# Optimization experiments

Measured on AMD Instinct MI355X. Metric: run time of the kernel, lower is better.

Reference implementation:

```python
import jax, jax.numpy as jnp
import numpy as np

N = 100000   # nodes
E = 1600000  # edges (avg degree 16)
F_IN, F_HID, F_OUT = 64, 64, 16


def setup_inputs() -> dict:
    key = jax.random.key(0)
    ks = jax.random.split(key, 10)
    features = jax.random.normal(ks[0], (N, F_IN), dtype=jnp.float32)
    src = jax.random.randint(ks[1], (E,), 0, N, dtype=jnp.int32)
    dst = jax.random.randint(ks[2], (E,), 0, N, dtype=jnp.int32)
    # Xavier-uniform weights, zero bias (matches nn.init in the module)
    def xavier(k, fan_in, fan_out):
        lim = np.sqrt(6.0 / (fan_in + fan_out))
        return jax.random.uniform(k, (fan_in, fan_out), jnp.float32, -lim, lim)
    return {
        "features": features,
        "W1": xavier(ks[3], F_IN, F_HID), "b1": jnp.zeros((F_HID,), jnp.float32),
        "W2": xavier(ks[4], F_HID, F_HID), "b2": jnp.zeros((F_HID,), jnp.float32),
        "W3": xavier(ks[5], F_HID, F_OUT), "b3": jnp.zeros((F_OUT,), jnp.float32),
        "src": src, "dst": dst,
    }


def pairnorm_scs(x):
    # PairNorm 'PN-SCS', scale=1
    col_mean = x.mean(axis=0)                                    # [F]
    rownorm = jnp.sqrt(1e-6 + jnp.sum(x * x, axis=1, keepdims=True))  # [N,1]
    return x / rownorm - col_mean


def graph_conv(h, src, dst, W, b):
    # copy_u('h','m') + sum reduce over edges, plus self-loop
    agg = jax.ops.segment_sum(h[src], dst, num_segments=N) + h   # [N,F]
    return agg @ W + b


def reference(features, W1, b1, W2, b2, W3, b3, src, dst):
    h = features
    for W, b in ((W1, b1), (W2, b2)):
        h = pairnorm_scs(h)
        h = jax.nn.relu(graph_conv(h, src, dst, W, b))
        # dropout p=0.0 -> identity
    return graph_conv(h, src, dst, W3, b3)
```

## Files before the change

kernel.cpp:

```cpp
#include <hip/hip_runtime.h>


#define NHB 64

__device__ __forceinline__ unsigned short f2bf(float f) {
  unsigned u = __builtin_bit_cast(unsigned, f);
  u += 0x7FFFu + ((u >> 16) & 1u);
  return (unsigned short)(u >> 16);
}
__device__ __forceinline__ float bf2f(unsigned short h) {
  return __builtin_bit_cast(float, ((unsigned)h) << 16);
}

__global__ __launch_bounds__(256) void prelude_kernel(
    const int* __restrict__ dst, int* __restrict__ cntA, int E,
    const float* __restrict__ x, float* __restrict__ cs, int n4) {
  __shared__ int lc[NHB];
  __shared__ float lds[16][64];
  const int t = threadIdx.x;
  if (t < NHB) lc[t] = 0;
  __syncthreads();
  const int stride = gridDim.x * blockDim.x;
  for (int e = blockIdx.x * blockDim.x + t; e < E; e += stride)
    atomicAdd(&lc[__builtin_nontemporal_load(&dst[e]) >> 11], 1);

  float s0 = 0.f, s1 = 0.f, s2 = 0.f, s3 = 0.f;
  for (int i = blockIdx.x * blockDim.x + t; i < n4; i += stride) {
    float4 v = ((const float4*)x)[i];
    s0 += v.x; s1 += v.y; s2 += v.z; s3 += v.w;
  }
  const int r = t >> 4;
  const int cq = (t & 15) * 4;
  lds[r][cq + 0] = s0; lds[r][cq + 1] = s1; lds[r][cq + 2] = s2; lds[r][cq + 3] = s3;
  __syncthreads();
  if (t < NHB && lc[t]) atomicAdd(&cntA[t], lc[t]);
  if (t < 64) {
    float tot = 0.f;
    #pragma unroll
    for (int rr = 0; rr < 16; ++rr) tot += lds[rr][t];
    unsafeAtomicAdd(&cs[t], tot);
  }
}

__global__ void colsum_kernel(const float* __restrict__ x, float* __restrict__ cs,
                              int n4) {
  __shared__ float lds[16][64];
  float s0 = 0.f, s1 = 0.f, s2 = 0.f, s3 = 0.f;
  const int t = threadIdx.x;
  const int stride = gridDim.x * blockDim.x;
  for (int i = blockIdx.x * blockDim.x + t; i < n4; i += stride) {
    float4 v = ((const float4*)x)[i];
    s0 += v.x; s1 += v.y; s2 += v.z; s3 += v.w;
  }
  const int r = t >> 4;
  const int cq = (t & 15) * 4;
  lds[r][cq + 0] = s0; lds[r][cq + 1] = s1; lds[r][cq + 2] = s2; lds[r][cq + 3] = s3;
  __syncthreads();
  if (t < 64) {
    float tot = 0.f;
    #pragma unroll
    for (int rr = 0; rr < 16; ++rr) tot += lds[rr][t];
    unsafeAtomicAdd(&cs[t], tot);
  }
}

__global__ __launch_bounds__(256) void matnorm_kernel(
    const float* x, const float* __restrict__ W,
    const float* __restrict__ cs, unsigned short* __restrict__ z,
    int N, float invN) {
  const int lane = threadIdx.x & 63;
  const int wid  = blockIdx.x * (blockDim.x >> 6) + (threadIdx.x >> 6);
  const int nw   = gridDim.x * (blockDim.x >> 6);

  float w[64];
  float cm = 0.f;
  #pragma unroll
  for (int k = 0; k < 64; ++k) {
    w[k] = W[k * 64 + lane];
    cm = fmaf(cs[k], w[k], cm);
  }
  cm *= invN;

  for (int row = wid; row < N; row += nw) {
    const float xv = x[(size_t)row * 64 + lane];
    float ss = xv * xv;
    #pragma unroll
    for (int m = 1; m < 64; m <<= 1) ss += __shfl_xor(ss, m, 64);
    const float rinv = 1.0f / sqrtf(1e-6f + ss);
    float acc = 0.f;
    #pragma unroll
    for (int k = 0; k < 64; ++k) {
      const float xk = __builtin_bit_cast(
          float, __builtin_amdgcn_readlane(__builtin_bit_cast(int, xv), k));
      acc = fmaf(xk, w[k], acc);
    }
    z[(size_t)row * 64 + lane] = f2bf(acc * rinv - cm);
  }
}

__global__ __launch_bounds__(256) void mat16_kernel(
    const float* __restrict__ x, const float* __restrict__ W3,
    unsigned short* __restrict__ z3, int N) {
  const int lane = threadIdx.x & 63;
  const int j = lane & 15;
  const int wid = blockIdx.x * (blockDim.x >> 6) + (threadIdx.x >> 6);
  const int nw  = gridDim.x * (blockDim.x >> 6);

  float w[64];
  #pragma unroll
  for (int k = 0; k < 64; ++k) w[k] = W3[k * 16 + j];
  for (int row = wid; row < N; row += nw) {
    const float xv = x[(size_t)row * 64 + lane];
    float acc = 0.f;
    #pragma unroll
    for (int k = 0; k < 64; ++k) {
      const float xk = __builtin_bit_cast(
          float, __builtin_amdgcn_readlane(__builtin_bit_cast(int, xv), k));
      acc = fmaf(xk, w[k], acc);
    }
    if (lane < 16) z3[(size_t)row * 16 + lane] = f2bf(acc);
  }
}


__global__ void scanA_kernel(const int* __restrict__ cntA,
                             int* __restrict__ baseA, int* __restrict__ curA,
                             int NHI) {
  if (threadIdx.x == 0) {
    int acc = 0;
    for (int p = 0; p < NHI; ++p) { baseA[p] = acc; curA[p] = acc; acc += cntA[p]; }
    baseA[NHI] = acc;
  }
}

#define TILE 2048
#define CAPA 96
__global__ __launch_bounds__(256) void scatterA_kernel(
    const int* __restrict__ src, const int* __restrict__ dst,
    int* __restrict__ curA, int* __restrict__ psrc, int* __restrict__ pdst,
    int E) {
  __shared__ int lss[NHB][CAPA], ldd[NHB][CAPA];
  __shared__ int lcnt[NHB], lbase[NHB];
  const int t = threadIdx.x;
  if (t < NHB) lcnt[t] = 0;
  __syncthreads();
  const int ntiles = (E + TILE - 1) / TILE;
  for (int tile = blockIdx.x; tile < ntiles; tile += gridDim.x) {
    const int base = tile * TILE;
    #pragma unroll
    for (int j = 0; j < TILE / 256; ++j) {
      const int e = base + j * 256 + t;
      if (e < E) {
        const int d = __builtin_nontemporal_load(&dst[e]);
        const int s = __builtin_nontemporal_load(&src[e]);
        const int p = d >> 11;
        const int slot = atomicAdd(&lcnt[p], 1);
        if (slot < CAPA) { lss[p][slot] = s; ldd[p][slot] = d; }
        else {
          const int pos = atomicAdd(&curA[p], 1);
          psrc[pos] = s; pdst[pos] = d;
        }
      }
    }
    __syncthreads();
    if (t < NHB) {
      int c = lcnt[t]; if (c > CAPA) c = CAPA;
      lbase[t] = c ? atomicAdd(&curA[t], c) : 0;
      lcnt[t] = c;
    }
    __syncthreads();
    for (int p = 0; p < NHB; ++p) {
      const int c = lcnt[p];
      if (t < c) {
        psrc[lbase[p] + t] = lss[p][t];
        pdst[lbase[p] + t] = ldd[p][t];
      }
    }
    __syncthreads();
    if (t < NHB) lcnt[t] = 0;
    __syncthreads();
  }
}

__global__ __launch_bounds__(1024) void fillsort_kernel(
    const int* __restrict__ psrc, const int* __restrict__ pdst,
    const int* __restrict__ baseA, int* __restrict__ rowstart,
    int* __restrict__ csr, int N, int E) {
  __shared__ int hist[2048];
  __shared__ int bs[1024];
  const int t = threadIdx.x;
  const int h = blockIdx.x;
  const int nlo = h << 11;
  const int elo = baseA[h], ehi = baseA[h + 1];

  for (int i = t; i < 2048; i += 1024) hist[i] = 0;
  __syncthreads();

  int e = elo + t;
  for (; e + 3 * 1024 < ehi; e += 4 * 1024) {
    const int d0 = pdst[e], d1 = pdst[e + 1024],
              d2 = pdst[e + 2048], d3 = pdst[e + 3072];
    atomicAdd(&hist[d0 - nlo], 1); atomicAdd(&hist[d1 - nlo], 1);
    atomicAdd(&hist[d2 - nlo], 1); atomicAdd(&hist[d3 - nlo], 1);
  }
  for (; e < ehi; e += 1024) atomicAdd(&hist[pdst[e] - nlo], 1);
  __syncthreads();

  const int c0 = hist[2 * t], c1 = hist[2 * t + 1];
  const int s = c0 + c1;
  bs[t] = s;
  __syncthreads();
  for (int off = 1; off < 1024; off <<= 1) {
    const int v = (t >= off) ? bs[t - off] : 0;
    __syncthreads();
    bs[t] += v;
    __syncthreads();
  }
  const int excl = bs[t] - s;

  const int n0 = nlo + 2 * t;
  hist[2 * t] = excl;
  hist[2 * t + 1] = excl + c0;
  if (n0 < N)     rowstart[n0]     = elo + excl;
  if (n0 + 1 < N) rowstart[n0 + 1] = elo + excl + c0;
  if (h == 0 && t == 0) rowstart[N] = E;
  __syncthreads();

  e = elo + t;
  for (; e + 3 * 1024 < ehi; e += 4 * 1024) {
    const int d0 = pdst[e],        s0 = psrc[e];
    const int d1 = pdst[e + 1024], s1 = psrc[e + 1024];
    const int d2 = pdst[e + 2048], s2 = psrc[e + 2048];
    const int d3 = pdst[e + 3072], s3 = psrc[e + 3072];
    csr[elo + atomicAdd(&hist[d0 - nlo], 1)] = s0;
    csr[elo + atomicAdd(&hist[d1 - nlo], 1)] = s1;
    csr[elo + atomicAdd(&hist[d2 - nlo], 1)] = s2;
    csr[elo + atomicAdd(&hist[d3 - nlo], 1)] = s3;
  }
  for (; e < ehi; e += 1024) {
    const int d = pdst[e], sv = psrc[e];
    csr[elo + atomicAdd(&hist[d - nlo], 1)] = sv;
  }
}

__global__ __launch_bounds__(256) void gather64_kernel(
    const unsigned short* __restrict__ z, const float* __restrict__ b,
    const int* __restrict__ rowstart, const int* __restrict__ csr,
    float* __restrict__ agg, int N) {
  const int lane = threadIdx.x & 63;
  int node = blockIdx.x * (blockDim.x >> 6) + (threadIdx.x >> 6);
  if (node >= N) return;
  node = __builtin_amdgcn_readfirstlane(node);
  const int start = rowstart[node];
  const int end   = rowstart[node + 1];
  const unsigned short hs = z[(size_t)node * 64 + lane];
  float a0 = 0.f, a1 = 0.f, a2 = 0.f, a3 = 0.f;
  int e = start;
  for (; e + 16 <= end; e += 16) {
    unsigned short h[16];
    #pragma unroll
    for (int j = 0; j < 16; ++j) h[j] = z[(size_t)csr[e + j] * 64 + lane];
    #pragma unroll
    for (int j = 0; j < 16; j += 4) {
      a0 += bf2f(h[j + 0]); a1 += bf2f(h[j + 1]);
      a2 += bf2f(h[j + 2]); a3 += bf2f(h[j + 3]);
    }
  }
  for (; e + 4 <= end; e += 4) {
    unsigned short h[4];
    #pragma unroll
    for (int j = 0; j < 4; ++j) h[j] = z[(size_t)csr[e + j] * 64 + lane];
    a0 += bf2f(h[0]); a1 += bf2f(h[1]); a2 += bf2f(h[2]); a3 += bf2f(h[3]);
  }
  for (; e < end; ++e) a0 += bf2f(z[(size_t)csr[e] * 64 + lane]);
  const float sum = (a0 + a1) + (a2 + a3);
  agg[(size_t)node * 64 + lane] = fmaxf(bf2f(hs) + b[lane] + sum, 0.f);
}

__global__ __launch_bounds__(256) void gather16_kernel(
    const unsigned short* __restrict__ z3, const float* __restrict__ b3,
    const int* __restrict__ rowstart, const int* __restrict__ csr,
    float* __restrict__ out, int N) {
  const int lane = threadIdx.x & 63;
  const int f = lane & 15;
  const int g = lane >> 4;
  int node = blockIdx.x * (blockDim.x >> 6) + (threadIdx.x >> 6);
  if (node >= N) return;
  node = __builtin_amdgcn_readfirstlane(node);
  const int start = rowstart[node];
  const int end   = rowstart[node + 1];
  float acc0 = 0.f, acc1 = 0.f;
  int e = start + g;
  for (; e + 4 < end; e += 8) {
    acc0 += bf2f(z3[(size_t)csr[e] * 16 + f]);
    acc1 += bf2f(z3[(size_t)csr[e + 4] * 16 + f]);
  }
  if (e < end) acc0 += bf2f(z3[(size_t)csr[e] * 16 + f]);
  float acc = acc0 + acc1;
  acc += __shfl_xor(acc, 16, 64);
  acc += __shfl_xor(acc, 32, 64);
  if (lane < 16)
    out[(size_t)node * 16 + f] = bf2f(z3[(size_t)node * 16 + f]) + b3[f] + acc;
}

extern "C" void kernel_launch(void* const* d_in, const int* in_sizes, int n_in,
                              void* d_out, int out_size, void* d_ws, size_t ws_size,
                              hipStream_t stream) {
  const float* feat = (const float*)d_in[0];
  const float* W1 = (const float*)d_in[1];
  const float* b1 = (const float*)d_in[2];
  const float* W2 = (const float*)d_in[3];
  const float* b2 = (const float*)d_in[4];
  const float* W3 = (const float*)d_in[5];
  const float* b3 = (const float*)d_in[6];
  const int* src = (const int*)d_in[7];
  const int* dst = (const int*)d_in[8];
  const int N = in_sizes[0] / 64;
  const int E = in_sizes[7];
  float* out = (float*)d_out;

  float* B            = (float*)d_ws;
  unsigned short* zb  = (unsigned short*)(B + (size_t)N * 64);
  unsigned short* z3b = zb + (size_t)N * 64;
  int* cntA  = (int*)(z3b + (size_t)N * 16);
  float* cs1 = (float*)(cntA + NHB);
  float* cs2 = cs1 + 64;
  int* baseA    = (int*)(cs2 + 64);
  int* curA     = baseA + NHB + 1;
  int* rowstart = curA + NHB;
  int* csr      = rowstart + N + 1;
  int* psrc = (int*)zb;
  int* pdst = psrc + E;

  const int NHI = (N + 2047) >> 11;
  const int node_blocks = (N + 3) / 4;
  const float invN = 1.0f / (float)N;

  hipMemsetAsync(cntA, 0, (NHB + 128) * sizeof(int), stream);
  prelude_kernel<<<512, 256, 0, stream>>>(dst, cntA, E, feat, cs1, N * 16);
  scanA_kernel<<<1, 64, 0, stream>>>(cntA, baseA, curA, NHI);
  scatterA_kernel<<<512, 256, 0, stream>>>(src, dst, curA, psrc, pdst, E);
  fillsort_kernel<<<NHI, 1024, 0, stream>>>(psrc, pdst, baseA, rowstart, csr, N, E);

  matnorm_kernel<<<1024, 256, 0, stream>>>(feat, W1, cs1, zb, N, invN);
  gather64_kernel<<<node_blocks, 256, 0, stream>>>(zb, b1, rowstart, csr, B, N);

  colsum_kernel<<<512, 256, 0, stream>>>(B, cs2, N * 16);
  matnorm_kernel<<<1024, 256, 0, stream>>>(B, W2, cs2, zb, N, invN);
  gather64_kernel<<<node_blocks, 256, 0, stream>>>(zb, b2, rowstart, csr, B, N);

  mat16_kernel<<<1024, 256, 0, stream>>>(B, W3, z3b, N);
  gather16_kernel<<<node_blocks, 256, 0, stream>>>(z3b, b3, rowstart, csr, out, N);
}
```

Before: 426.0 us.

## Fuse layer-1 aggregation with layer-2 normalize/matmul and pack edge keys

The column-mean correction is moved out of the pre-aggregation term and applied after aggregation as degree+1 times (mean·W), which lets each layer's gather kernel also do the next layer's row normalization and matmul. The separate colsum, matnorm and mat16 passes disappear, and so do the fp32 intermediate writes and reads. The edge partition also packs src and the low dst bits into one 32-bit word, halving scatter traffic. In exchange the fused kernels reload W from global per node, and the packing assumes src fits in 21 bits.

Measured after the change: 524.1 us. 1.23x slower.

```diff
diff --git a/kernel.cpp b/kernel.cpp
--- a/kernel.cpp
+++ b/kernel.cpp
@@ -42,44 +42,33 @@
   }
 }
 
-__global__ void colsum_kernel(const float* __restrict__ x, float* __restrict__ cs,
-                              int n4) {
-  __shared__ float lds[16][64];
-  float s0 = 0.f, s1 = 0.f, s2 = 0.f, s3 = 0.f;
+__global__ void scanA_kernel(const int* __restrict__ cntA,
+                             int* __restrict__ baseA, int* __restrict__ curA,
+                             const float* __restrict__ cs1,
+                             const float* __restrict__ W1,
+                             float* __restrict__ cmW1, int NHI, float invN) {
   const int t = threadIdx.x;
-  const int stride = gridDim.x * blockDim.x;
-  for (int i = blockIdx.x * blockDim.x + t; i < n4; i += stride) {
-    float4 v = ((const float4*)x)[i];
-    s0 += v.x; s1 += v.y; s2 += v.z; s3 += v.w;
-  }
-  const int r = t >> 4;
-  const int cq = (t & 15) * 4;
-  lds[r][cq + 0] = s0; lds[r][cq + 1] = s1; lds[r][cq + 2] = s2; lds[r][cq + 3] = s3;
-  __syncthreads();
-  if (t < 64) {
-    float tot = 0.f;
-    #pragma unroll
-    for (int rr = 0; rr < 16; ++rr) tot += lds[rr][t];
-    unsafeAtomicAdd(&cs[t], tot);
-  }
+  if (t == 0) {
+    int acc = 0;
+    for (int p = 0; p < NHI; ++p) { baseA[p] = acc; curA[p] = acc; acc += cntA[p]; }
+    baseA[NHI] = acc;
+  }
+  float cm = 0.f;
+  #pragma unroll
+  for (int k = 0; k < 64; ++k) cm = fmaf(cs1[k], W1[k * 64 + t], cm);
+  cmW1[t] = cm * invN;
 }
 
 __global__ __launch_bounds__(256) void matnorm_kernel(
-    const float* x, const float* __restrict__ W,
-    const float* __restrict__ cs, unsigned short* __restrict__ z,
-    int N, float invN) {
+    const float* __restrict__ x, const float* __restrict__ W,
+    unsigned short* __restrict__ z, int N) {
   const int lane = threadIdx.x & 63;
   const int wid  = blockIdx.x * (blockDim.x >> 6) + (threadIdx.x >> 6);
   const int nw   = gridDim.x * (blockDim.x >> 6);
 
   float w[64];
-  float cm = 0.f;
   #pragma unroll
-  for (int k = 0; k < 64; ++k) {
-    w[k] = W[k * 64 + lane];
-    cm = fmaf(cs[k], w[k], cm);
-  }
-  cm *= invN;
+  for (int k = 0; k < 64; ++k) w[k] = W[k * 64 + lane];
 
   for (int row = wid; row < N; row += nw) {
     const float xv = x[(size_t)row * 64 + lane];
@@ -94,52 +83,17 @@
           float, __builtin_amdgcn_readlane(__builtin_bit_cast(int, xv), k));
       acc = fmaf(xk, w[k], acc);
     }
-    z[(size_t)row * 64 + lane] = f2bf(acc * rinv - cm);
-  }
-}
-
-__global__ __launch_bounds__(256) void mat16_kernel(
-    const float* __restrict__ x, const float* __restrict__ W3,
-    unsigned short* __restrict__ z3, int N) {
-  const int lane = threadIdx.x & 63;
-  const int j = lane & 15;
-  const int wid = blockIdx.x * (blockDim.x >> 6) + (threadIdx.x >> 6);
-  const int nw  = gridDim.x * (blockDim.x >> 6);
-
-  float w[64];
-  #pragma unroll
-  for (int k = 0; k < 64; ++k) w[k] = W3[k * 16 + j];
-  for (int row = wid; row < N; row += nw) {
-    const float xv = x[(size_t)row * 64 + lane];
-    float acc = 0.f;
-    #pragma unroll
-    for (int k = 0; k < 64; ++k) {
-      const float xk = __builtin_bit_cast(
-          float, __builtin_amdgcn_readlane(__builtin_bit_cast(int, xv), k));
-      acc = fmaf(xk, w[k], acc);
-    }
-    if (lane < 16) z3[(size_t)row * 16 + lane] = f2bf(acc);
-  }
-}
-
-
-__global__ void scanA_kernel(const int* __restrict__ cntA,
-                             int* __restrict__ baseA, int* __restrict__ curA,
-                             int NHI) {
-  if (threadIdx.x == 0) {
-    int acc = 0;
-    for (int p = 0; p < NHI; ++p) { baseA[p] = acc; curA[p] = acc; acc += cntA[p]; }
-    baseA[NHI] = acc;
-  }
-}
+    z[(size_t)row * 64 + lane] = f2bf(acc * rinv);
+  }
+}
+
 
 #define TILE 2048
 #define CAPA 96
 __global__ __launch_bounds__(256) void scatterA_kernel(
     const int* __restrict__ src, const int* __restrict__ dst,
-    int* __restrict__ curA, int* __restrict__ psrc, int* __restrict__ pdst,
-    int E) {
-  __shared__ int lss[NHB][CAPA], ldd[NHB][CAPA];
+    int* __restrict__ curA, unsigned* __restrict__ ppack, int E) {
+  __shared__ unsigned lpk[NHB][CAPA];
   __shared__ int lcnt[NHB], lbase[NHB];
   const int t = threadIdx.x;
   if (t < NHB) lcnt[t] = 0;
@@ -153,13 +107,11 @@
       if (e < E) {
         const int d = __builtin_nontemporal_load(&dst[e]);
         const int s = __builtin_nontemporal_load(&src[e]);
+        const unsigned pw = ((unsigned)s << 11) | ((unsigned)d & 2047u);
         const int p = d >> 11;
         const int slot = atomicAdd(&lcnt[p], 1);
-        if (slot < CAPA) { lss[p][slot] = s; ldd[p][slot] = d; }
-        else {
-          const int pos = atomicAdd(&curA[p], 1);
-          psrc[pos] = s; pdst[pos] = d;
-        }
+        if (slot < CAPA) lpk[p][slot] = pw;
+        else ppack[atomicAdd(&curA[p], 1)] = pw;
       }
     }
     __syncthreads();
@@ -171,10 +123,7 @@
     __syncthreads();
     for (int p = 0; p < NHB; ++p) {
       const int c = lcnt[p];
-      if (t < c) {
-        psrc[lbase[p] + t] = lss[p][t];
-        pdst[lbase[p] + t] = ldd[p][t];
-      }
+      if (t < c) ppack[lbase[p] + t] = lpk[p][t];
     }
     __syncthreads();
     if (t < NHB) lcnt[t] = 0;
@@ -183,9 +132,8 @@
 }
 
 __global__ __launch_bounds__(1024) void fillsort_kernel(
-    const int* __restrict__ psrc, const int* __restrict__ pdst,
-    const int* __restrict__ baseA, int* __restrict__ rowstart,
-    int* __restrict__ csr, int N, int E) {
+    const unsigned* __restrict__ ppack, const int* __restrict__ baseA,
+    int* __restrict__ rowstart, int* __restrict__ csr, int N, int E) {
   __shared__ int hist[2048];
   __shared__ int bs[1024];
   const int t = threadIdx.x;
@@ -198,12 +146,12 @@
 
   int e = elo + t;
   for (; e + 3 * 1024 < ehi; e += 4 * 1024) {
-    const int d0 = pdst[e], d1 = pdst[e + 1024],
-              d2 = pdst[e + 2048], d3 = pdst[e + 3072];
-    atomicAdd(&hist[d0 - nlo], 1); atomicAdd(&hist[d1 - nlo], 1);
-    atomicAdd(&hist[d2 - nlo], 1); atomicAdd(&hist[d3 - nlo], 1);
-  }
-  for (; e < ehi; e += 1024) atomicAdd(&hist[pdst[e] - nlo], 1);
+    const unsigned p0 = ppack[e], p1 = ppack[e + 1024],
+                   p2 = ppack[e + 2048], p3 = ppack[e + 3072];
+    atomicAdd(&hist[p0 & 2047u], 1); atomicAdd(&hist[p1 & 2047u], 1);
+    atomicAdd(&hist[p2 & 2047u], 1); atomicAdd(&hist[p3 & 2047u], 1);
+  }
+  for (; e < ehi; e += 1024) atomicAdd(&hist[ppack[e] & 2047u], 1);
   __syncthreads();
 
   const int c0 = hist[2 * t], c1 = hist[2 * t + 1];
@@ -228,38 +176,102 @@
 
   e = elo + t;
   for (; e + 3 * 1024 < ehi; e += 4 * 1024) {
-    const int d0 = pdst[e],        s0 = psrc[e];
-    const int d1 = pdst[e + 1024], s1 = psrc[e + 1024];
-    const int d2 = pdst[e + 2048], s2 = psrc[e + 2048];
-    const int d3 = pdst[e + 3072], s3 = psrc[e + 3072];
-    csr[elo + atomicAdd(&hist[d0 - nlo], 1)] = s0;
-    csr[elo + atomicAdd(&hist[d1 - nlo], 1)] = s1;
-    csr[elo + atomicAdd(&hist[d2 - nlo], 1)] = s2;
-    csr[elo + atomicAdd(&hist[d3 - nlo], 1)] = s3;
+    const unsigned p0 = ppack[e],        p1 = ppack[e + 1024];
+    const unsigned p2 = ppack[e + 2048], p3 = ppack[e + 3072];
+    csr[elo + atomicAdd(&hist[p0 & 2047u], 1)] = (int)(p0 >> 11);
+    csr[elo + atomicAdd(&hist[p1 & 2047u], 1)] = (int)(p1 >> 11);
+    csr[elo + atomicAdd(&hist[p2 & 2047u], 1)] = (int)(p2 >> 11);
+    csr[elo + atomicAdd(&hist[p3 & 2047u], 1)] = (int)(p3 >> 11);
   }
   for (; e < ehi; e += 1024) {
-    const int d = pdst[e], sv = psrc[e];
-    csr[elo + atomicAdd(&hist[d - nlo], 1)] = sv;
-  }
-}
-
-__global__ __launch_bounds__(256) void gather64_kernel(
-    const unsigned short* __restrict__ z, const float* __restrict__ b,
+    const unsigned p = ppack[e];
+    csr[elo + atomicAdd(&hist[p & 2047u], 1)] = (int)(p >> 11);
+  }
+}
+
+__global__ __launch_bounds__(1024) void gather_l1_kernel(
+    const unsigned short* __restrict__ z1, const float* __restrict__ W2,
+    const float* __restrict__ b1, const float* __restrict__ cmW1,
     const int* __restrict__ rowstart, const int* __restrict__ csr,
-    float* __restrict__ agg, int N) {
+    unsigned short* __restrict__ z2, float* __restrict__ cs2, int N) {
+  const int lane = threadIdx.x & 63;
+  const int w = threadIdx.x >> 6;
+  const int node = blockIdx.x * 16 + w;
+  float o = 0.f;
+  if (node < N) {
+    const int nd = __builtin_amdgcn_readfirstlane(node);
+    const int start = rowstart[nd];
+    const int end   = rowstart[nd + 1];
+    const unsigned short hs = z1[(size_t)nd * 64 + lane];
+    float a0 = 0.f, a1 = 0.f, a2 = 0.f, a3 = 0.f;
+    int e = start;
+    for (; e + 16 <= end; e += 16) {
+      unsigned short h[16];
+      #pragma unroll
+      for (int j = 0; j < 16; ++j) h[j] = z1[(size_t)csr[e + j] * 64 + lane];
+      #pragma unroll
+      for (int j = 0; j < 16; j += 4) {
+        a0 += bf2f(h[j + 0]); a1 += bf2f(h[j + 1]);
+        a2 += bf2f(h[j + 2]); a3 += bf2f(h[j + 3]);
+      }
+    }
+    for (; e + 4 <= end; e += 4) {
+      unsigned short h[4];
+      #pragma unroll
+      for (int j = 0; j < 4; ++j) h[j] = z1[(size_t)csr[e + j] * 64 + lane];
+      a0 += bf2f(h[0]); a1 += bf2f(h[1]); a2 += bf2f(h[2]); a3 += bf2f(h[3]);
+    }
+    for (; e < end; ++e) a0 += bf2f(z1[(size_t)csr[e] * 64 + lane]);
+    const float sum = (a0 + a1) + (a2 + a3);
+    const float degp1 = (float)(end - start + 1);
+    o = fmaxf(bf2f(hs) + b1[lane] + sum - degp1 * cmW1[lane], 0.f);
+    float ss = o * o;
+    #pragma unroll
+    for (int m = 1; m < 64; m <<= 1) ss += __shfl_xor(ss, m, 64);
+    const float rinv = 1.0f / sqrtf(1e-6f + ss);
+    float acc = 0.f;
+    #pragma unroll
+    for (int k = 0; k < 64; ++k) {
+      const float ok = __builtin_bit_cast(
+          float, __builtin_amdgcn_readlane(__builtin_bit_cast(int, o), k));
+      acc = fmaf(ok, W2[k * 64 + lane], acc);
+    }
+    z2[(size_t)nd * 64 + lane] = f2bf(acc * rinv);
+  }
+  __shared__ float lcs[16][64];
+  lcs[w][lane] = o;
+  __syncthreads();
+  if (threadIdx.x < 64) {
+    float tot = 0.f;
+    #pragma unroll
+    for (int r = 0; r < 16; ++r) tot += lcs[r][threadIdx.x];
+    unsafeAtomicAdd(&cs2[threadIdx.x], tot);
+  }
+}
+
+__global__ __launch_bounds__(256) void gather_l2_kernel(
+    const unsigned short* __restrict__ z2, const float* __restrict__ W2,
+    const float* __restrict__ cs2, const float* __restrict__ b2,
+    const float* __restrict__ W3, const int* __restrict__ rowstart,
+    const int* __restrict__ csr, unsigned short* __restrict__ z3,
+    int N, float invN) {
   const int lane = threadIdx.x & 63;
   int node = blockIdx.x * (blockDim.x >> 6) + (threadIdx.x >> 6);
   if (node >= N) return;
   node = __builtin_amdgcn_readfirstlane(node);
+  float cm = 0.f;
+  #pragma unroll
+  for (int k = 0; k < 64; ++k) cm = fmaf(cs2[k], W2[k * 64 + lane], cm);
+  cm *= invN;
   const int start = rowstart[node];
   const int end   = rowstart[node + 1];
-  const unsigned short hs = z[(size_t)node * 64 + lane];
+  const unsigned short hs = z2[(size_t)node * 64 + lane];
   float a0 = 0.f, a1 = 0.f, a2 = 0.f, a3 = 0.f;
   int e = start;
   for (; e + 16 <= end; e += 16) {
     unsigned short h[16];
     #pragma unroll
-    for (int j = 0; j < 16; ++j) h[j] = z[(size_t)csr[e + j] * 64 + lane];
+    for (int j = 0; j < 16; ++j) h[j] = z2[(size_t)csr[e + j] * 64 + lane];
     #pragma unroll
     for (int j = 0; j < 16; j += 4) {
       a0 += bf2f(h[j + 0]); a1 += bf2f(h[j + 1]);
@@ -269,12 +281,22 @@
   for (; e + 4 <= end; e += 4) {
     unsigned short h[4];
     #pragma unroll
-    for (int j = 0; j < 4; ++j) h[j] = z[(size_t)csr[e + j] * 64 + lane];
+    for (int j = 0; j < 4; ++j) h[j] = z2[(size_t)csr[e + j] * 64 + lane];
     a0 += bf2f(h[0]); a1 += bf2f(h[1]); a2 += bf2f(h[2]); a3 += bf2f(h[3]);
   }
-  for (; e < end; ++e) a0 += bf2f(z[(size_t)csr[e] * 64 + lane]);
+  for (; e < end; ++e) a0 += bf2f(z2[(size_t)csr[e] * 64 + lane]);
   const float sum = (a0 + a1) + (a2 + a3);
-  agg[(size_t)node * 64 + lane] = fmaxf(bf2f(hs) + b[lane] + sum, 0.f);
+  const float degp1 = (float)(end - start + 1);
+  const float o = fmaxf(bf2f(hs) + b2[lane] + sum - degp1 * cm, 0.f);
+  const int j = lane & 15;
+  float acc = 0.f;
+  #pragma unroll
+  for (int k = 0; k < 64; ++k) {
+    const float ok = __builtin_bit_cast(
+        float, __builtin_amdgcn_readlane(__builtin_bit_cast(int, o), k));
+    acc = fmaf(ok, W3[k * 16 + j], acc);
+  }
+  if (lane < 16) z3[(size_t)node * 16 + lane] = f2bf(acc);
 }
 
 __global__ __launch_bounds__(256) void gather16_kernel(
@@ -319,36 +341,35 @@
   const int E = in_sizes[7];
   float* out = (float*)d_out;
 
-  float* B            = (float*)d_ws;
-  unsigned short* zb  = (unsigned short*)(B + (size_t)N * 64);
-  unsigned short* z3b = zb + (size_t)N * 64;
+  unsigned short* z1b = (unsigned short*)d_ws;
+  unsigned short* z2b = z1b + (size_t)N * 64;
+  unsigned short* z3b = z2b + (size_t)N * 64;
   int* cntA  = (int*)(z3b + (size_t)N * 16);
   float* cs1 = (float*)(cntA + NHB);
   float* cs2 = cs1 + 64;
-  int* baseA    = (int*)(cs2 + 64);
+  float* cmW1   = cs2 + 64;
+  int* baseA    = (int*)(cmW1 + 64);
   int* curA     = baseA + NHB + 1;
   int* rowstart = curA + NHB;
   int* csr      = rowstart + N + 1;
-  int* psrc = (int*)zb;
-  int* pdst = psrc + E;
+  unsigned* ppack = (unsigned*)z2b;
 
   const int NHI = (N + 2047) >> 11;
   const int node_blocks = (N + 3) / 4;
+  const int l1_blocks   = (N + 15) / 16;
   const float invN = 1.0f / (float)N;
 
   hipMemsetAsync(cntA, 0, (NHB + 128) * sizeof(int), stream);
   prelude_kernel<<<512, 256, 0, stream>>>(dst, cntA, E, feat, cs1, N * 16);
-  scanA_kernel<<<1, 64, 0, stream>>>(cntA, baseA, curA, NHI);
-  scatterA_kernel<<<512, 256, 0, stream>>>(src, dst, curA, psrc, pdst, E);
-  fillsort_kernel<<<NHI, 1024, 0, stream>>>(psrc, pdst, baseA, rowstart, csr, N, E);
-
-  matnorm_kernel<<<1024, 256, 0, stream>>>(feat, W1, cs1, zb, N, invN);
-  gather64_kernel<<<node_blocks, 256, 0, stream>>>(zb, b1, rowstart, csr, B, N);
-
-  colsum_kernel<<<512, 256, 0, stream>>>(B, cs2, N * 16);
-  matnorm_kernel<<<1024, 256, 0, stream>>>(B, W2, cs2, zb, N, invN);
-  gather64_kernel<<<node_blocks, 256, 0, stream>>>(zb, b2, rowstart, csr, B, N);
-
-  mat16_kernel<<<1024, 256, 0, stream>>>(B, W3, z3b, N);
+  scanA_kernel<<<1, 64, 0, stream>>>(cntA, baseA, curA, cs1, W1, cmW1, NHI, invN);
+  scatterA_kernel<<<512, 256, 0, stream>>>(src, dst, curA, ppack, E);
+  fillsort_kernel<<<NHI, 1024, 0, stream>>>(ppack, baseA, rowstart, csr, N, E);
+
+  matnorm_kernel<<<1024, 256, 0, stream>>>(feat, W1, z1b, N);
+
+  gather_l1_kernel<<<l1_blocks, 1024, 0, stream>>>(z1b, W2, b1, cmW1,
+                                                   rowstart, csr, z2b, cs2, N);
+  gather_l2_kernel<<<node_blocks, 256, 0, stream>>>(z2b, W2, cs2, b2, W3,
+                                                    rowstart, csr, z3b, N, invN);
   gather16_kernel<<<node_blocks, 256, 0, stream>>>(z3b, b3, rowstart, csr, out, N);
 }
```

## Pack edge src/dst into one word and fuse layer-3 matmul into gather

Applied to the files above, without the earlier changes.

Edge binning now uses 1024-node buckets, so the low 10 bits of dst fit alongside src in a single 32-bit word. This halves the scatter and fillsort traffic and the shared staging. Separately, the layer-2 gather now computes the 64x16 W3 projection in-register, which removes the mat16 kernel and the fp32 write and re-read of the layer-2 activations. The cost is more buckets and fillsort blocks, and per-node readlane matmul work inside the gather.

New measurement: 409.9 us. -3.8%, faster.

```diff
diff --git a/kernel.cpp b/kernel.cpp
--- a/kernel.cpp
+++ b/kernel.cpp
@@ -1,7 +1,7 @@
 #include <hip/hip_runtime.h>
 
 
-#define NHB 64
+#define NHB 128
 
 __device__ __forceinline__ unsigned short f2bf(float f) {
   unsigned u = __builtin_bit_cast(unsigned, f);
@@ -22,7 +22,7 @@
   __syncthreads();
   const int stride = gridDim.x * blockDim.x;
   for (int e = blockIdx.x * blockDim.x + t; e < E; e += stride)
-    atomicAdd(&lc[__builtin_nontemporal_load(&dst[e]) >> 11], 1);
+    atomicAdd(&lc[__builtin_nontemporal_load(&dst[e]) >> 10], 1);
 
   float s0 = 0.f, s1 = 0.f, s2 = 0.f, s3 = 0.f;
   for (int i = blockIdx.x * blockDim.x + t; i < n4; i += stride) {
@@ -98,30 +98,6 @@
   }
 }
 
-__global__ __launch_bounds__(256) void mat16_kernel(
-    const float* __restrict__ x, const float* __restrict__ W3,
-    unsigned short* __restrict__ z3, int N) {
-  const int lane = threadIdx.x & 63;
-  const int j = lane & 15;
-  const int wid = blockIdx.x * (blockDim.x >> 6) + (threadIdx.x >> 6);
-  const int nw  = gridDim.x * (blockDim.x >> 6);
-
-  float w[64];
-  #pragma unroll
-  for (int k = 0; k < 64; ++k) w[k] = W3[k * 16 + j];
-  for (int row = wid; row < N; row += nw) {
-    const float xv = x[(size_t)row * 64 + lane];
-    float acc = 0.f;
-    #pragma unroll
-    for (int k = 0; k < 64; ++k) {
-      const float xk = __builtin_bit_cast(
-          float, __builtin_amdgcn_readlane(__builtin_bit_cast(int, xv), k));
-      acc = fmaf(xk, w[k], acc);
-    }
-    if (lane < 16) z3[(size_t)row * 16 + lane] = f2bf(acc);
-  }
-}
-
 
 __global__ void scanA_kernel(const int* __restrict__ cntA,
                              int* __restrict__ baseA, int* __restrict__ curA,
@@ -134,12 +110,11 @@
 }
 
 #define TILE 2048
-#define CAPA 96
+#define CAPA 48
 __global__ __launch_bounds__(256) void scatterA_kernel(
     const int* __restrict__ src, const int* __restrict__ dst,
-    int* __restrict__ curA, int* __restrict__ psrc, int* __restrict__ pdst,
-    int E) {
-  __shared__ int lss[NHB][CAPA], ldd[NHB][CAPA];
+    int* __restrict__ curA, unsigned* __restrict__ ppack, int E) {
+  __shared__ unsigned lpk[NHB][CAPA];
   __shared__ int lcnt[NHB], lbase[NHB];
   const int t = threadIdx.x;
   if (t < NHB) lcnt[t] = 0;
@@ -153,13 +128,11 @@
       if (e < E) {
         const int d = __builtin_nontemporal_load(&dst[e]);
         const int s = __builtin_nontemporal_load(&src[e]);
-        const int p = d >> 11;
+        const unsigned pw = ((unsigned)s << 10) | ((unsigned)d & 1023u);
+        const int p = d >> 10;
         const int slot = atomicAdd(&lcnt[p], 1);
-        if (slot < CAPA) { lss[p][slot] = s; ldd[p][slot] = d; }
-        else {
-          const int pos = atomicAdd(&curA[p], 1);
-          psrc[pos] = s; pdst[pos] = d;
-        }
+        if (slot < CAPA) lpk[p][slot] = pw;
+        else ppack[atomicAdd(&curA[p], 1)] = pw;
       }
     }
     __syncthreads();
@@ -171,10 +144,7 @@
     __syncthreads();
     for (int p = 0; p < NHB; ++p) {
       const int c = lcnt[p];
-      if (t < c) {
-        psrc[lbase[p] + t] = lss[p][t];
-        pdst[lbase[p] + t] = ldd[p][t];
-      }
+      if (t < c) ppack[lbase[p] + t] = lpk[p][t];
     }
     __syncthreads();
     if (t < NHB) lcnt[t] = 0;
@@ -183,32 +153,30 @@
 }
 
 __global__ __launch_bounds__(1024) void fillsort_kernel(
-    const int* __restrict__ psrc, const int* __restrict__ pdst,
-    const int* __restrict__ baseA, int* __restrict__ rowstart,
-    int* __restrict__ csr, int N, int E) {
-  __shared__ int hist[2048];
+    const unsigned* __restrict__ ppack, const int* __restrict__ baseA,
+    int* __restrict__ rowstart, int* __restrict__ csr, int N, int E) {
+  __shared__ int hist[1024];
   __shared__ int bs[1024];
   const int t = threadIdx.x;
   const int h = blockIdx.x;
-  const int nlo = h << 11;
+  const int nlo = h << 10;
   const int elo = baseA[h], ehi = baseA[h + 1];
 
-  for (int i = t; i < 2048; i += 1024) hist[i] = 0;
+  hist[t] = 0;
   __syncthreads();
 
   int e = elo + t;
   for (; e + 3 * 1024 < ehi; e += 4 * 1024) {
-    const int d0 = pdst[e], d1 = pdst[e + 1024],
-              d2 = pdst[e + 2048], d3 = pdst[e + 3072];
-    atomicAdd(&hist[d0 - nlo], 1); atomicAdd(&hist[d1 - nlo], 1);
-    atomicAdd(&hist[d2 - nlo], 1); atomicAdd(&hist[d3 - nlo], 1);
-  }
-  for (; e < ehi; e += 1024) atomicAdd(&hist[pdst[e] - nlo], 1);
-  __syncthreads();
-
-  const int c0 = hist[2 * t], c1 = hist[2 * t + 1];
-  const int s = c0 + c1;
-  bs[t] = s;
+    const unsigned p0 = ppack[e], p1 = ppack[e + 1024],
+                   p2 = ppack[e + 2048], p3 = ppack[e + 3072];
+    atomicAdd(&hist[p0 & 1023u], 1); atomicAdd(&hist[p1 & 1023u], 1);
+    atomicAdd(&hist[p2 & 1023u], 1); atomicAdd(&hist[p3 & 1023u], 1);
+  }
+  for (; e < ehi; e += 1024) atomicAdd(&hist[ppack[e] & 1023u], 1);
+  __syncthreads();
+
+  const int c = hist[t];
+  bs[t] = c;
   __syncthreads();
   for (int off = 1; off < 1024; off <<= 1) {
     const int v = (t >= off) ? bs[t - off] : 0;
@@ -216,30 +184,26 @@
     bs[t] += v;
     __syncthreads();
   }
-  const int excl = bs[t] - s;
-
-  const int n0 = nlo + 2 * t;
-  hist[2 * t] = excl;
-  hist[2 * t + 1] = excl + c0;
-  if (n0 < N)     rowstart[n0]     = elo + excl;
-  if (n0 + 1 < N) rowstart[n0 + 1] = elo + excl + c0;
+  const int excl = bs[t] - c;
+
+  hist[t] = excl;
+  const int n0 = nlo + t;
+  if (n0 < N) rowstart[n0] = elo + excl;
   if (h == 0 && t == 0) rowstart[N] = E;
   __syncthreads();
 
   e = elo + t;
   for (; e + 3 * 1024 < ehi; e += 4 * 1024) {
-    const int d0 = pdst[e],        s0 = psrc[e];
-    const int d1 = pdst[e + 1024], s1 = psrc[e + 1024];
-    const int d2 = pdst[e + 2048], s2 = psrc[e + 2048];
-    const int d3 = pdst[e + 3072], s3 = psrc[e + 3072];
-    csr[elo + atomicAdd(&hist[d0 - nlo], 1)] = s0;
-    csr[elo + atomicAdd(&hist[d1 - nlo], 1)] = s1;
-    csr[elo + atomicAdd(&hist[d2 - nlo], 1)] = s2;
-    csr[elo + atomicAdd(&hist[d3 - nlo], 1)] = s3;
+    const unsigned p0 = ppack[e],        p1 = ppack[e + 1024];
+    const unsigned p2 = ppack[e + 2048], p3 = ppack[e + 3072];
+    csr[elo + atomicAdd(&hist[p0 & 1023u], 1)] = (int)(p0 >> 10);
+    csr[elo + atomicAdd(&hist[p1 & 1023u], 1)] = (int)(p1 >> 10);
+    csr[elo + atomicAdd(&hist[p2 & 1023u], 1)] = (int)(p2 >> 10);
+    csr[elo + atomicAdd(&hist[p3 & 1023u], 1)] = (int)(p3 >> 10);
   }
   for (; e < ehi; e += 1024) {
-    const int d = pdst[e], sv = psrc[e];
-    csr[elo + atomicAdd(&hist[d - nlo], 1)] = sv;
+    const unsigned p = ppack[e];
+    csr[elo + atomicAdd(&hist[p & 1023u], 1)] = (int)(p >> 10);
   }
 }
 
@@ -275,6 +239,49 @@
   for (; e < end; ++e) a0 += bf2f(z[(size_t)csr[e] * 64 + lane]);
   const float sum = (a0 + a1) + (a2 + a3);
   agg[(size_t)node * 64 + lane] = fmaxf(bf2f(hs) + b[lane] + sum, 0.f);
+}
+
+__global__ __launch_bounds__(256) void gather_l2_kernel(
+    const unsigned short* __restrict__ z2, const float* __restrict__ b2,
+    const float* __restrict__ W3, const int* __restrict__ rowstart,
+    const int* __restrict__ csr, unsigned short* __restrict__ z3, int N) {
+  const int lane = threadIdx.x & 63;
+  int node = blockIdx.x * (blockDim.x >> 6) + (threadIdx.x >> 6);
+  if (node >= N) return;
+  node = __builtin_amdgcn_readfirstlane(node);
+  const int start = rowstart[node];
+  const int end   = rowstart[node + 1];
+  const unsigned short hs = z2[(size_t)node * 64 + lane];
+  float a0 = 0.f, a1 = 0.f, a2 = 0.f, a3 = 0.f;
+  int e = start;
+  for (; e + 16 <= end; e += 16) {
+    unsigned short h[16];
+    #pragma unroll
+    for (int j = 0; j < 16; ++j) h[j] = z2[(size_t)csr[e + j] * 64 + lane];
+    #pragma unroll
+    for (int j = 0; j < 16; j += 4) {
+      a0 += bf2f(h[j + 0]); a1 += bf2f(h[j + 1]);
+      a2 += bf2f(h[j + 2]); a3 += bf2f(h[j + 3]);
+    }
+  }
+  for (; e + 4 <= end; e += 4) {
+    unsigned short h[4];
+    #pragma unroll
+    for (int j = 0; j < 4; ++j) h[j] = z2[(size_t)csr[e + j] * 64 + lane];
+    a0 += bf2f(h[0]); a1 += bf2f(h[1]); a2 += bf2f(h[2]); a3 += bf2f(h[3]);
+  }
+  for (; e < end; ++e) a0 += bf2f(z2[(size_t)csr[e] * 64 + lane]);
+  const float sum = (a0 + a1) + (a2 + a3);
+  const float o = fmaxf(bf2f(hs) + b2[lane] + sum, 0.f);
+  const int j = lane & 15;
+  float acc = 0.f;
+  #pragma unroll
+  for (int k = 0; k < 64; ++k) {
+    const float ok = __builtin_bit_cast(
+        float, __builtin_amdgcn_readlane(__builtin_bit_cast(int, o), k));
+    acc = fmaf(ok, W3[k * 16 + j], acc);
+  }
+  if (lane < 16) z3[(size_t)node * 16 + lane] = f2bf(acc);
 }
 
 __global__ __launch_bounds__(256) void gather16_kernel(
@@ -329,26 +336,25 @@
   int* curA     = baseA + NHB + 1;
   int* rowstart = curA + NHB;
   int* csr      = rowstart + N + 1;
-  int* psrc = (int*)zb;
-  int* pdst = psrc + E;
-
-  const int NHI = (N + 2047) >> 11;
+  unsigned* ppack = (unsigned*)zb;
+
+  const int NHI = (N + 1023) >> 10;
   const int node_blocks = (N + 3) / 4;
   const float invN = 1.0f / (float)N;
 
   hipMemsetAsync(cntA, 0, (NHB + 128) * sizeof(int), stream);
   prelude_kernel<<<512, 256, 0, stream>>>(dst, cntA, E, feat, cs1, N * 16);
   scanA_kernel<<<1, 64, 0, stream>>>(cntA, baseA, curA, NHI);
-  scatterA_kernel<<<512, 256, 0, stream>>>(src, dst, curA, psrc, pdst, E);
-  fillsort_kernel<<<NHI, 1024, 0, stream>>>(psrc, pdst, baseA, rowstart, csr, N, E);
+  scatterA_kernel<<<512, 256, 0, stream>>>(src, dst, curA, ppack, E);
+  fillsort_kernel<<<NHI, 1024, 0, stream>>>(ppack, baseA, rowstart, csr, N, E);
 
   matnorm_kernel<<<1024, 256, 0, stream>>>(feat, W1, cs1, zb, N, invN);
   gather64_kernel<<<node_blocks, 256, 0, stream>>>(zb, b1, rowstart, csr, B, N);
 
   colsum_kernel<<<512, 256, 0, stream>>>(B, cs2, N * 16);
   matnorm_kernel<<<1024, 256, 0, stream>>>(B, W2, cs2, zb, N, invN);
-  gather64_kernel<<<node_blocks, 256, 0, stream>>>(zb, b2, rowstart, csr, B, N);
-
-  mat16_kernel<<<1024, 256, 0, stream>>>(B, W3, z3b, N);
+  gather_l2_kernel<<<node_blocks, 256, 0, stream>>>(zb, b2, W3, rowstart, csr,
+                                                    z3b, N);
+
   gather16_kernel<<<node_blocks, 256, 0, stream>>>(z3b, b3, rowstart, csr, out, N);
 }
```
